# Kernel tuning notes

Measured on AMD Instinct MI355X. Metric: run time of the kernel, lower is better.

The kernel has to match this reference:

```python
import jax, jax.numpy as jnp
import numpy as np

B, TI, TE, B_IN, B_OUT = 1024, 2, 3, 16, 32
DEGREES = (0, 2, 4, 6, 8)  # symmetric=True, l_in=8


def setup_inputs() -> dict:
    key = jax.random.key(0)
    ks = jax.random.split(key, 2 * len(DEGREES))
    inp = {}
    for i, l in enumerate(DEGREES):
        nsh = 2 * l + 1
        inp[f"x{l}"] = jax.random.normal(ks[2 * i], (B, TI, TE, B_IN, nsh), dtype=jnp.float32)
        inp[f"w{l}"] = jax.random.uniform(ks[2 * i + 1], (TI, TE, B_IN, B_OUT, nsh), dtype=jnp.float32) * 0.1
    inp["bias"] = jnp.zeros((1, TI, TE, B_OUT, 1, 1), dtype=jnp.float32)
    return inp


def reference(x0, x2, x4, x6, x8, w0, w2, w4, w6, w8, bias):
    xs = {0: x0, 2: x2, 4: x4, 6: x6, 8: x8}
    ws = {0: w0, 2: w2, 4: w4, 6: w6, 8: w8}
    rh = []
    for l in DEGREES:
        # (n,a,b,i,l) x (a,b,i,o,k) -> (n,a,b,o,l,k)
        out = jnp.einsum('nabil,abiok->nabolk', xs[l], ws[l])
        if l == 0:
            out = out + bias
        rh.append(out)
    return tuple(rh)
```

## Files before the change

### kernel.cpp

```cpp
#include <hip/hip_runtime.h>

#define B_    1024
#define AB_   6
#define BIN_  16
#define BOUT_ 32

typedef float f4 __attribute__((ext_vector_type(4)));
typedef _Float16 hlf4 __attribute__((ext_vector_type(4)));

#define SOFTBAR()                                                  \
    do {                                                           \
        asm volatile("s_waitcnt lgkmcnt(0)" ::: "memory");         \
        __builtin_amdgcn_s_barrier();                              \
        __builtin_amdgcn_sched_barrier(0);                         \
    } while (0)

template<int NSH, int OH, int SPB>
__device__ __forceinline__ void mfma_lds_body(const float* __restrict__ X,
                                              const float* __restrict__ W,
                                              float* __restrict__ OUT,
                                              float* os, int b) {
    constexpr int OPB  = BOUT_ / OH;
    constexpr int SZ   = BIN_ * NSH;
    constexpr int NOUT = BOUT_ * NSH * NSH;
    constexpr int USZ  = OPB * NSH * NSH;
    constexpr int NTU  = (OPB * NSH) / 16;
    constexpr int MT   = (NSH + 15) / 16;
    constexpr int NTQ  = (NTU + 3) / 4;

    const int tid  = threadIdx.x;
    const int lane = tid & 63;
    const int w    = tid >> 6;
    const int lm   = lane & 15;
    const int lk   = (lane >> 4) * 4;

    const int h  = (OH == 2) ? (b & 1) : 0;
    const int gi = (OH == 2) ? (b >> 1) : b;
    const int ab = gi % AB_;
    const int g  = gi / AB_;

    const float* Wab = W + (size_t)ab * (BIN_ * BOUT_ * NSH);

    hlf4 bfrag[NTQ];
#pragma unroll
    for (int t = 0; t < NTQ; ++t) {
        const int ni = w * NTQ + t;
        if (ni < NTU) {
            const int n = h * (OPB * NSH) + ni * 16 + lm;
#pragma unroll
            for (int j = 0; j < 4; ++j)
                bfrag[t][j] = (_Float16)Wab[(lk + j) * (BOUT_ * NSH) + n];
        }
    }

    auto load_a = [&](int slice, hlf4* dst) {
        const float* Xs = X + (size_t)slice * SZ;
#pragma unroll
        for (int mi = 0; mi < MT; ++mi) {
            const int l  = mi * 16 + lm;
            const int lc = (l > NSH - 1) ? (NSH - 1) : l;
#pragma unroll
            for (int j = 0; j < 4; ++j)
                dst[mi][j] = (_Float16)Xs[(lk + j) * NSH + lc];
        }
    };

    hlf4 acur[MT], anext[MT];
    load_a(ab + AB_ * (g * SPB), acur);

    for (int s = 0; s < SPB; ++s) {
        const int slice = ab + AB_ * (g * SPB + s);

#pragma unroll
        for (int t = 0; t < NTQ; ++t) {
            const int ni = w * NTQ + t;
            if (ni < NTU) {
                const int nl = ni * 16 + lm;
                const int ol = nl / NSH;
                const int kq = nl - ol * NSH;
                float* base = os + ol * (NSH * NSH) + kq;
#pragma unroll
                for (int mi = 0; mi < MT; ++mi) {
                    f4 d = __builtin_amdgcn_mfma_f32_16x16x16f16(
                        acur[mi], bfrag[t], (f4){0.f, 0.f, 0.f, 0.f}, 0, 0, 0);
#pragma unroll
                    for (int j = 0; j < 4; ++j) {
                        const int l = mi * 16 + lk + j;
                        if (l < NSH) base[l * NSH] = d[j];
                    }
                }
            }
        }
        SOFTBAR();

        if (s + 1 < SPB) load_a(slice + AB_, anext);

        f4* dst = (f4*)(OUT + (size_t)slice * NOUT + (size_t)h * USZ);
        const f4* src = (const f4*)os;
        for (int c = tid; c < USZ / 4; c += 256) dst[c] = src[c];
        SOFTBAR();

#pragma unroll
        for (int mi = 0; mi < MT; ++mi) acur[mi] = anext[mi];
    }
}

__device__ __forceinline__ void l0_body(const float* __restrict__ X,
                                        const float* __restrict__ W,
                                        const float* __restrict__ bias,
                                        float* __restrict__ OUT, int b) {
    const int o  = threadIdx.x & 31;
    const int ns = threadIdx.x >> 5;
    const int n0 = (b / AB_) * 64;
    const int ab = b % AB_;
    float wv[BIN_];
#pragma unroll
    for (int i = 0; i < BIN_; ++i) wv[i] = W[(ab * BIN_ + i) * BOUT_ + o];
    const float bv = bias[ab * BOUT_ + o];
#pragma unroll
    for (int s = 0; s < 8; ++s) {
        const int n = n0 + ns + s * 8;
        const float* Xp = X + ((size_t)n * AB_ + ab) * BIN_;
        float acc = bv;
#pragma unroll
        for (int i = 0; i < BIN_; ++i) acc = fmaf(Xp[i], wv[i], acc);
        OUT[((size_t)n * AB_ + ab) * BOUT_ + o] = acc;
    }
}

#define NB8 1536
#define NB6 1536
#define NB4 768
#define NB2 768
#define NB0 96

__global__ __launch_bounds__(256, 4)
void s2conv_one(const float* __restrict__ x0, const float* __restrict__ x2,
                const float* __restrict__ x4, const float* __restrict__ x6,
                const float* __restrict__ x8,
                const float* __restrict__ w0, const float* __restrict__ w2,
                const float* __restrict__ w4, const float* __restrict__ w6,
                const float* __restrict__ w8,
                const float* __restrict__ bias, float* __restrict__ out,
                size_t off0, size_t off2, size_t off4, size_t off6, size_t off8) {
    __shared__ __attribute__((aligned(16))) float os[16 * 17 * 17];
    int b = blockIdx.x;
    if (b < NB8) { mfma_lds_body<17, 2, 8>(x8, w8, out + off8, os, b); return; }
    b -= NB8;
    if (b < NB6) { mfma_lds_body<13, 2, 8>(x6, w6, out + off6, os, b); return; }
    b -= NB6;
    if (b < NB4) { mfma_lds_body< 9, 1, 8>(x4, w4, out + off4, os, b); return; }
    b -= NB4;
    if (b < NB2) { mfma_lds_body< 5, 1, 8>(x2, w2, out + off2, os, b); return; }
    b -= NB2;
    l0_body(x0, w0, bias, out + off0, b);
}

extern "C" void kernel_launch(void* const* d_in, const int* in_sizes, int n_in,
                              void* d_out, int out_size, void* d_ws, size_t ws_size,
                              hipStream_t stream) {
    const float* x0 = (const float*)d_in[0];
    const float* w0 = (const float*)d_in[1];
    const float* x2 = (const float*)d_in[2];
    const float* w2 = (const float*)d_in[3];
    const float* x4 = (const float*)d_in[4];
    const float* w4 = (const float*)d_in[5];
    const float* x6 = (const float*)d_in[6];
    const float* w6 = (const float*)d_in[7];
    const float* x8 = (const float*)d_in[8];
    const float* w8 = (const float*)d_in[9];
    const float* bias = (const float*)d_in[10];
    float* out = (float*)d_out;

    const size_t per = (size_t)B_ * AB_ * BOUT_;
    size_t off0 = 0;
    size_t off2 = off0 + per * 1;
    size_t off4 = off2 + per * 25;
    size_t off6 = off4 + per * 81;
    size_t off8 = off6 + per * 169;

    const int nblocks = NB8 + NB6 + NB4 + NB2 + NB0;
    s2conv_one<<<nblocks, 256, 0, stream>>>(x0, x2, x4, x6, x8,
                                            w0, w2, w4, w6, w8,
                                            bias, out,
                                            off0, off2, off4, off6, off8);
}
```

Measured before the change: 106.8 us.

## Batch multiple slices per LDS round and cut block counts per degree

```diff
diff --git a/kernel.cpp b/kernel.cpp
--- a/kernel.cpp
+++ b/kernel.cpp
@@ -15,7 +15,7 @@
         __builtin_amdgcn_sched_barrier(0);                         \
     } while (0)
 
-template<int NSH, int OH, int SPB>
+template<int NSH, int OH, int G, int SPB>
 __device__ __forceinline__ void mfma_lds_body(const float* __restrict__ X,
                                               const float* __restrict__ W,
                                               float* __restrict__ OUT,
@@ -27,6 +27,8 @@
     constexpr int NTU  = (OPB * NSH) / 16;
     constexpr int MT   = (NSH + 15) / 16;
     constexpr int NTQ  = (NTU + 3) / 4;
+    constexpr int NG   = SPB / G;
+    static_assert(SPB % G == 0, "group geometry");
 
     const int tid  = threadIdx.x;
     const int lane = tid & 63;
@@ -37,7 +39,8 @@
     const int h  = (OH == 2) ? (b & 1) : 0;
     const int gi = (OH == 2) ? (b >> 1) : b;
     const int ab = gi % AB_;
-    const int g  = gi / AB_;
+    const int gb = gi / AB_;
+    const int t0 = gb * SPB;
 
     const float* Wab = W + (size_t)ab * (BIN_ * BOUT_ * NSH);
 
@@ -53,55 +56,66 @@
         }
     }
 
-    auto load_a = [&](int slice, hlf4* dst) {
-        const float* Xs = X + (size_t)slice * SZ;
-#pragma unroll
-        for (int mi = 0; mi < MT; ++mi) {
-            const int l  = mi * 16 + lm;
-            const int lc = (l > NSH - 1) ? (NSH - 1) : l;
-#pragma unroll
-            for (int j = 0; j < 4; ++j)
-                dst[mi][j] = (_Float16)Xs[(lk + j) * NSH + lc];
+    auto load_group = [&](int ng, hlf4 (*dst)[MT]) {
+#pragma unroll
+        for (int g = 0; g < G; ++g) {
+            const float* Xs = X + (size_t)(ab + AB_ * (t0 + ng * G + g)) * SZ;
+#pragma unroll
+            for (int mi = 0; mi < MT; ++mi) {
+                const int l  = mi * 16 + lm;
+                const int lc = (l > NSH - 1) ? (NSH - 1) : l;
+#pragma unroll
+                for (int j = 0; j < 4; ++j)
+                    dst[g][mi][j] = (_Float16)Xs[(lk + j) * NSH + lc];
+            }
         }
     };
 
-    hlf4 acur[MT], anext[MT];
-    load_a(ab + AB_ * (g * SPB), acur);
-
-    for (int s = 0; s < SPB; ++s) {
-        const int slice = ab + AB_ * (g * SPB + s);
-
-#pragma unroll
-        for (int t = 0; t < NTQ; ++t) {
-            const int ni = w * NTQ + t;
-            if (ni < NTU) {
-                const int nl = ni * 16 + lm;
-                const int ol = nl / NSH;
-                const int kq = nl - ol * NSH;
-                float* base = os + ol * (NSH * NSH) + kq;
-#pragma unroll
-                for (int mi = 0; mi < MT; ++mi) {
-                    f4 d = __builtin_amdgcn_mfma_f32_16x16x16f16(
-                        acur[mi], bfrag[t], (f4){0.f, 0.f, 0.f, 0.f}, 0, 0, 0);
-#pragma unroll
-                    for (int j = 0; j < 4; ++j) {
-                        const int l = mi * 16 + lk + j;
-                        if (l < NSH) base[l * NSH] = d[j];
+    hlf4 acur[G][MT], anext[G][MT];
+    load_group(0, acur);
+
+    for (int ng = 0; ng < NG; ++ng) {
+#pragma unroll
+        for (int g = 0; g < G; ++g) {
+            float* buf = os + g * USZ;
+#pragma unroll
+            for (int t = 0; t < NTQ; ++t) {
+                const int ni = w * NTQ + t;
+                if (ni < NTU) {
+                    const int nl = ni * 16 + lm;
+                    const int ol = nl / NSH;
+                    const int kq = nl - ol * NSH;
+                    float* base = buf + ol * (NSH * NSH) + kq;
+#pragma unroll
+                    for (int mi = 0; mi < MT; ++mi) {
+                        f4 d = __builtin_amdgcn_mfma_f32_16x16x16f16(
+                            acur[g][mi], bfrag[t], (f4){0.f, 0.f, 0.f, 0.f}, 0, 0, 0);
+#pragma unroll
+                        for (int j = 0; j < 4; ++j) {
+                            const int l = mi * 16 + lk + j;
+                            if (l < NSH) base[l * NSH] = d[j];
+                        }
                     }
                 }
             }
         }
         SOFTBAR();
 
-        if (s + 1 < SPB) load_a(slice + AB_, anext);
-
-        f4* dst = (f4*)(OUT + (size_t)slice * NOUT + (size_t)h * USZ);
-        const f4* src = (const f4*)os;
-        for (int c = tid; c < USZ / 4; c += 256) dst[c] = src[c];
+        if (ng + 1 < NG) load_group(ng + 1, anext);
+
+#pragma unroll
+        for (int g = 0; g < G; ++g) {
+            f4* dst = (f4*)(OUT + (size_t)(ab + AB_ * (t0 + ng * G + g)) * NOUT
+                            + (size_t)h * USZ);
+            const f4* src = (const f4*)(os + g * USZ);
+            for (int c = tid; c < USZ / 4; c += 256) dst[c] = src[c];
+        }
         SOFTBAR();
 
 #pragma unroll
-        for (int mi = 0; mi < MT; ++mi) acur[mi] = anext[mi];
+        for (int g = 0; g < G; ++g)
+#pragma unroll
+            for (int mi = 0; mi < MT; ++mi) acur[g][mi] = anext[g][mi];
     }
 }
 
@@ -128,10 +142,10 @@
     }
 }
 
-#define NB8 1536
-#define NB6 1536
-#define NB4 768
-#define NB2 768
+#define NB8 768
+#define NB6 384
+#define NB4 384
+#define NB2 192
 #define NB0 96
 
 __global__ __launch_bounds__(256, 4)
@@ -143,15 +157,15 @@
                 const float* __restrict__ w8,
                 const float* __restrict__ bias, float* __restrict__ out,
                 size_t off0, size_t off2, size_t off4, size_t off6, size_t off8) {
-    __shared__ __attribute__((aligned(16))) float os[16 * 17 * 17];
+    __shared__ __attribute__((aligned(16))) float os[BOUT_ * 13 * 13];
     int b = blockIdx.x;
-    if (b < NB8) { mfma_lds_body<17, 2, 8>(x8, w8, out + off8, os, b); return; }
+    if (b < NB8) { mfma_lds_body<17, 2, 1, 16>(x8, w8, out + off8, os, b); return; }
     b -= NB8;
-    if (b < NB6) { mfma_lds_body<13, 2, 8>(x6, w6, out + off6, os, b); return; }
+    if (b < NB6) { mfma_lds_body<13, 1, 1, 16>(x6, w6, out + off6, os, b); return; }
     b -= NB6;
-    if (b < NB4) { mfma_lds_body< 9, 1, 8>(x4, w4, out + off4, os, b); return; }
+    if (b < NB4) { mfma_lds_body< 9, 1, 2, 16>(x4, w4, out + off4, os, b); return; }
     b -= NB4;
-    if (b < NB2) { mfma_lds_body< 5, 1, 8>(x2, w2, out + off2, os, b); return; }
+    if (b < NB2) { mfma_lds_body< 5, 1, 4, 32>(x2, w2, out + off2, os, b); return; }
     b -= NB2;
     l0_body(x0, w0, bias, out + off0, b);
 }
```

Result: no change. 107.8 us (+1.0%).
